# Performance work log

Measured on AMD Instinct MI355X. Metric: run time of the kernel, lower is better.

## Reference

```python
import jax, jax.numpy as jnp
import numpy as np

B = 1024
D = 128  # in_out_dim


def _lin(k, i, o):
    return jax.random.normal(k, (i, o), jnp.float32) / np.sqrt(i)


def setup_inputs() -> dict:
    key = jax.random.key(0)
    ks = jax.random.split(key, 24)
    inp = {
        'pseudo_t': jax.random.uniform(ks[0], (), jnp.float32),
        'x': jax.random.normal(ks[1], (B, D), jnp.float32),
        'g_x': jax.random.normal(ks[2], (B, 1), jnp.float32),
        'p': jax.random.uniform(ks[3], (B, 1), jnp.float32),
        # GRN encoder: 128->1024->960->896 (Tanh), decoder 896->128
        'gw0': _lin(ks[4], 128, 1024), 'gb0': jnp.zeros((1024,), jnp.float32),
        'gw1': _lin(ks[5], 1024, 960), 'gb1': jnp.zeros((960,), jnp.float32),
        'gw2': _lin(ks[6], 960, 896), 'gb2': jnp.zeros((896,), jnp.float32),
        'gdw': _lin(ks[7], 896, 128), 'gdb': jnp.zeros((128,), jnp.float32),
        # BRD encoder: 129->512->448 (Tanh), decoder 448->1
        'bw0': _lin(ks[8], 129, 512), 'bb0': jnp.zeros((512,), jnp.float32),
        'bw1': _lin(ks[9], 512, 448), 'bb1': jnp.zeros((448,), jnp.float32),
        'bdw': _lin(ks[10], 448, 1), 'bdb': jnp.zeros((1,), jnp.float32),
    }
    return inp


def reference(pseudo_t, x, g_x, p, gw0, gb0, gw1, gb1, gw2, gb2, gdw, gdb,
              bw0, bb0, bw1, bb1, bdw, bdb):
    bsz = x.shape[0]
    x_gene = x[:, :-1]                       # [B, D-1]
    s = jnp.full((bsz, 1), pseudo_t, x.dtype)

    def grn(state):                          # [..., D] -> [..., D]
        h = jnp.tanh(state @ gw0 + gb0)
        h = jnp.tanh(h @ gw1 + gb1)
        h = jnp.tanh(h @ gw2 + gb2)
        return h @ gdw + gdb

    dx_dt = grn(jnp.concatenate([s, x_gene], axis=1))   # [B, D]

    # BRD growth function g(x, t)
    st = jnp.concatenate([s, x], axis=1)                # [B, D+1]
    e = jnp.tanh(st @ bw0 + bb0)
    e = jnp.tanh(e @ bw1 + bb1)
    g = e @ bdw + bdb                                   # [B, 1]

    # trace of d(dx_dt[:, :D-1]) / d(x_gene), per sample (CNF divergence)
    s_scalar = jnp.reshape(pseudo_t, (1,)).astype(x.dtype)

    def f_single(xg_i):                                 # [D-1] -> [D]
        return grn(jnp.concatenate([s_scalar, xg_i]))

    jac = jax.vmap(jax.jacfwd(f_single))(x_gene)        # [B, D, D-1]
    tr = jnp.trace(jac[:, :D - 1, :], axis1=1, axis2=2) # [B]

    dp_dt = g - p * tr[:, None]                         # [B, 1]
    return (dx_dt, g, dp_dt)
```

## Files before the change

kernel.cpp:

```cpp
#include <hip/hip_runtime.h>


typedef __bf16 bf16;
typedef __bf16 bf16x8 __attribute__((ext_vector_type(8)));
typedef float floatx4 __attribute__((ext_vector_type(4)));

#if defined(__has_builtin)
#if __has_builtin(__builtin_amdgcn_global_load_lds)
#define HAVE_GLL 1
#endif
#endif

typedef __attribute__((address_space(3))) char lds_char_t;
typedef __attribute__((address_space(1))) const char gbl_char_t;

__device__ inline void async_load16(const void* gp, void* lp) {
#ifdef HAVE_GLL
  __builtin_amdgcn_global_load_lds((gbl_char_t*)gp, (lds_char_t*)lp, 16, 0, 0);
#else
  *(bf16x8*)lp = *(const bf16x8*)gp;
#endif
}

__device__ inline void stage_async(const bf16* src, long row0, int ld, int kc,
                                   bf16* dst, int wid, int sr8, int cph) {
#pragma unroll
  for (int t = 0; t < 4; ++t) {
    const int r = (wid * 4 + t) * 8 + sr8;
    const int csrc = (cph - r) & 7;
    async_load16(src + (row0 + r) * (size_t)ld + kc + csrc * 8,
                 dst + r * 64 + cph * 8);
  }
}

__device__ inline void mfma_block(const bf16* As, const bf16* Bs,
                                  floatx4 (&acc)[4][4], int wm, int wn,
                                  int l16, int quad) {
#pragma unroll
  for (int ks = 0; ks < 2; ++ks) {
    bf16x8 af[4], bfv[4];
#pragma unroll
    for (int mt = 0; mt < 4; ++mt) {
      const int r = wm * 64 + mt * 16 + l16;
      const int c = (ks * 4 + quad + r) & 7;
      af[mt] = *(const bf16x8*)(As + r * 64 + c * 8);
    }
#pragma unroll
    for (int nt = 0; nt < 4; ++nt) {
      const int r = wn * 64 + nt * 16 + l16;
      const int c = (ks * 4 + quad + r) & 7;
      bfv[nt] = *(const bf16x8*)(Bs + r * 64 + c * 8);
    }
#pragma unroll
    for (int mt = 0; mt < 4; ++mt)
#pragma unroll
      for (int nt = 0; nt < 4; ++nt)
        acc[mt][nt] = __builtin_amdgcn_mfma_f32_16x16x32_bf16(af[mt], bfv[nt], acc[mt][nt], 0, 0, 0);
  }
}

__device__ inline void g0_body(bf16* G0, const bf16* gw0b, const bf16* d0b,
                               int i0, int ch, int b, int tid) {
  const int nb = ((b >> 9) << 3) + (b & 7);
  const int inner = (b >> 3) & 63;
  if (nb >= ch) return;
  const int e = inner * 256 + tid;
  const int d = e >> 7;
  const int j = (e & 127) << 3;
  const int ig = i0 + nb;
  const int wsel = (d + 1 < 128) ? d + 1 : 127;
  bf16x8 gv = *(const bf16x8*)(gw0b + wsel * 1024 + j);
  bf16x8 dv = *(const bf16x8*)(d0b + (size_t)ig * 1024 + j);
  bf16x8 v;
#pragma unroll
  for (int k = 0; k < 8; ++k) v[k] = (bf16)((float)gv[k] * (float)dv[k]);
  *(bf16x8*)(G0 + ((size_t)nb * 128 + d) * 1024 + j) = v;
}

struct T8 {
  const bf16* A;
  const bf16* Bm;
  const bf16* sc;
  bf16* Upr;
  const float* gdw;
  float* tr;
  int i0, NT, ch, nTiles;
  int chn, i0n;
  bf16* G0;
  const bf16* gw0b;
  const bf16* d0b;
};

__device__ __forceinline__ void gemm256(const bf16* Aop, const bf16* Bop,
                                        int m0, int n0, int NT, char* lds,
                                        floatx4 (&acc)[8][4]) {
  const int tid = threadIdx.x;
  const int wid = tid >> 6, lane = tid & 63;
  const int wm = wid & 1, wn = wid >> 1;
  const int quad = lane >> 4, l16 = lane & 15;

  const int sr = tid >> 2;
  const int sg = tid & 3;
  const int gs = sg ^ (sr & 3);
  const bf16* aS0 = Aop + (size_t)(m0 + sr) * 1024 + gs * 8;
  const bf16* aS1 = aS0 + (size_t)128 * 1024;
  const bf16* bS0 = Bop + (size_t)(n0 + sr) * 1024 + gs * 8;
  const bf16* bS1 = bS0 + (size_t)128 * 1024;
  const int dO0 = tid * 16, dO1 = 8192 + tid * 16;

  const int fsw = (quad ^ (l16 & 3)) * 8;
  const int fo  = (wm * 128 + l16) * 32 + fsw;
  const int fob = (wn * 64  + l16) * 32 + fsw;

#define STAGE_PAIR(tt, ss)                                                     \
  {                                                                            \
    char* db = lds + (((tt) & 1) * 65536) + ((ss) * 16384);                    \
    const int kc = (tt) * 64 + (ss) * 32;                                      \
    async_load16(aS0 + kc, db + dO0);                                          \
    async_load16(aS1 + kc, db + dO1);                                          \
    async_load16(bS0 + kc, db + 32768 + dO0);                                  \
    async_load16(bS1 + kc, db + 32768 + dO1);                                  \
  }

#define PHASE(T, S, DOSTAGE, ST, SS, VMSEL)                                    \
  {                                                                            \
    const bf16* Af = (const bf16*)(lds + ((T) & 1) * 65536 + (S) * 16384) + fo;\
    const bf16* Bf = (const bf16*)(lds + ((T) & 1) * 65536 + 32768 +           \
                                   (S) * 16384) + fob;                         \
    bf16x8 af[8], bv[4];                                                       \
    _Pragma("unroll")                                                          \
    for (int mf = 0; mf < 8; ++mf) af[mf] = *(const bf16x8*)(Af + mf * 512);   \
    _Pragma("unroll")                                                          \
    for (int nf = 0; nf < 4; ++nf) bv[nf] = *(const bf16x8*)(Bf + nf * 512);   \
    if (DOSTAGE) STAGE_PAIR(ST, SS);                                           \
    __builtin_amdgcn_sched_barrier(0);                                         \
    {                                                                          \
      const int vms = (VMSEL);                                                 \
      if (vms == 8)      asm volatile("s_waitcnt vmcnt(8)");                   \
      else if (vms == 4) asm volatile("s_waitcnt vmcnt(4)");                   \
      else if (vms == 0) asm volatile("s_waitcnt vmcnt(0)");                   \
    }                                                                          \
    __builtin_amdgcn_sched_barrier(0);                                         \
    __builtin_amdgcn_s_setprio(1);                                             \
    _Pragma("unroll")                                                          \
    for (int mf = 0; mf < 8; ++mf)                                             \
      _Pragma("unroll")                                                        \
      for (int nf = 0; nf < 4; ++nf)                                           \
        acc[mf][nf] = __builtin_amdgcn_mfma_f32_16x16x32_bf16(                 \
            af[mf], bv[nf], acc[mf][nf], 0, 0, 0);                             \
    __builtin_amdgcn_s_setprio(0);                                             \
    asm volatile("s_waitcnt lgkmcnt(0)");                                      \
    __builtin_amdgcn_sched_barrier(0);                                         \
    __builtin_amdgcn_s_barrier();                                              \
    __builtin_amdgcn_sched_barrier(0);                                         \
  }

  STAGE_PAIR(0, 0);
  STAGE_PAIR(0, 1);
  STAGE_PAIR(1, 0);
  __builtin_amdgcn_sched_barrier(0);
  asm volatile("s_waitcnt vmcnt(8)");
  __builtin_amdgcn_sched_barrier(0);
  __builtin_amdgcn_s_barrier();
  __builtin_amdgcn_sched_barrier(0);

#pragma unroll 2
  for (int t = 0; t < NT; ++t) {
    PHASE(t, 0, (t + 1 < NT), t + 1, 1, (t + 1 < NT) ? 8 : 0);
    PHASE(t, 1, (t + 2 < NT), t + 2, 0,
          (t + 2 < NT) ? 8 : ((t + 1 < NT) ? 4 : -1));
  }
#undef PHASE
#undef STAGE_PAIR
}

__global__ __launch_bounds__(512, 2) void kt8_b1(T8 p) {
  extern __shared__ __align__(16) char lds[];
  const int mt = (blockIdx.x >> 3) & 3;
  const int nt = ((blockIdx.x >> 5) << 3) | (blockIdx.x & 7);
  if (nt >= p.nTiles) return;

  floatx4 acc[8][4];
#pragma unroll
  for (int a = 0; a < 8; ++a)
#pragma unroll
    for (int b = 0; b < 4; ++b)
#pragma unroll
      for (int r = 0; r < 4; ++r) acc[a][b][r] = 0.0f;

  gemm256(p.A, p.Bm, mt * 256, nt * 256, p.NT, lds, acc);

  const int tid = threadIdx.x;
  const int wid = tid >> 6, lane = tid & 63;
  const int wm = wid & 1, wn = wid >> 1;
  const int quad = lane >> 4, l16 = lane & 15;
  const long nLim = (long)p.ch * 128;
  const int mb = mt * 256 + wm * 128;

#pragma unroll
  for (int nf = 0; nf < 4; ++nf) {
    const long n = (long)nt * 256 + wn * 64 + nf * 16 + l16;
    if (n < nLim) {
      const int ig = p.i0 + (int)(n >> 7);
      const bf16* dp = p.sc + (size_t)ig * 960;
      bf16* urow = p.Upr + (size_t)n * 1024;
#pragma unroll
      for (int mf = 0; mf < 8; ++mf) {
        const int mg = mb + mf * 16 + quad * 4;
        if (mg < 960) {
          union { bf16 h[4]; uint2 u; } o;
#pragma unroll
          for (int r = 0; r < 4; ++r)
            o.h[r] = (bf16)(acc[mf][nf][r] * (float)dp[mg + r]);
          *(uint2*)(urow + mg) = o.u;
        }
      }
    }
  }
}

__global__ __launch_bounds__(512, 2) void kt8_b2(T8 p) {
  extern __shared__ __align__(16) char lds[];
  const int mt = (blockIdx.x >> 3) & 3;
  const int nt = ((blockIdx.x >> 5) << 3) | (blockIdx.x & 7);
  const int tid = threadIdx.x;

  if (nt < p.nTiles) {
    floatx4 acc[8][4];
#pragma unroll
    for (int a = 0; a < 8; ++a)
#pragma unroll
      for (int b = 0; b < 4; ++b)
#pragma unroll
        for (int r = 0; r < 4; ++r) acc[a][b][r] = 0.0f;

    gemm256(p.A, p.Bm, mt * 256, nt * 256, p.NT, lds, acc);

    const int wid = tid >> 6, lane = tid & 63;
    const int wm = wid & 1, wn = wid >> 1;
    const int quad = lane >> 4, l16 = lane & 15;
    const long nLim = (long)p.ch * 128;
    const int mb = mt * 256 + wm * 128;

    float s = 0.0f;
#pragma unroll
    for (int nf = 0; nf < 4; ++nf) {
      const long n = (long)nt * 256 + wn * 64 + nf * 16 + l16;
      const int d = (int)(n & 127);
      if (n < nLim && d < 127) {
        const int ig = p.i0 + (int)(n >> 7);
        const bf16* dp = p.sc + (size_t)ig * 896;
#pragma unroll
        for (int mf = 0; mf < 8; ++mf) {
          const int mg = mb + mf * 16 + quad * 4;
          if (mg < 896) {
#pragma unroll
            for (int r = 0; r < 4; ++r) {
              const float w = (float)dp[mg + r] * p.gdw[(mg + r) * 128 + d];
              s += acc[mf][nf][r] * w;
            }
          }
        }
      }
    }
#pragma unroll
    for (int off = 1; off < 64; off <<= 1) s += __shfl_xor(s, off, 64);
    float* red = (float*)lds;
    if (lane == 0) red[wid] = s;
    __syncthreads();
    const int igA = p.i0 + nt * 2;
    if (tid == 0)
      atomicAdd(p.tr + igA, red[0] + red[1] + red[2] + red[3]);
    if (tid == 256 && nt * 2 + 1 < p.ch)
      atomicAdd(p.tr + igA + 1, red[4] + red[5] + red[6] + red[7]);
  }

  if (p.chn > 0) {
    const size_t V = (size_t)p.chn * 16384;
    for (size_t v = (size_t)blockIdx.x * 512 + tid; v < V;
         v += (size_t)gridDim.x * 512) {
      const int j = ((int)(v & 127)) << 3;
      const size_t rest = v >> 7;
      const int d = (int)(rest & 127);
      const int nb = (int)(rest >> 7);
      const int wsel = (d + 1 < 128) ? d + 1 : 127;
      bf16x8 gv = *(const bf16x8*)(p.gw0b + wsel * 1024 + j);
      bf16x8 dv = *(const bf16x8*)(p.d0b + (size_t)(p.i0n + nb) * 1024 + j);
      bf16x8 o;
#pragma unroll
      for (int k = 0; k < 8; ++k) o[k] = (bf16)((float)gv[k] * (float)dv[k]);
      *(bf16x8*)(p.G0 + ((size_t)nb * 128 + d) * 1024 + j) = o;
    }
  }
}

struct FArgs {
  const bf16* A; int lda;
  const bf16* Bt; int ldb;
  const float* bias;
  bf16* C; int ldc;
  bf16* D; int ldd;
  float* outF; int ldo;
  int K; int realN; int gridX;
};

template <int ACT>
__device__ inline void fwd_body(const FArgs& p, int bx, bf16* As, bf16* Bs) {
  const int tid  = threadIdx.x;
  const int wid  = tid >> 6, lane = tid & 63;
  const int wm   = wid & 1, wn = wid >> 1;
  const int quad = lane >> 4, l16 = lane & 15;
  const int sr8  = lane >> 3, cph = lane & 7;
  const int m0   = (bx % p.gridX) * 128;
  const int bn0  = (bx / p.gridX) * 128;

  floatx4 acc[4][4];
#pragma unroll
  for (int a = 0; a < 4; ++a)
#pragma unroll
    for (int b = 0; b < 4; ++b)
#pragma unroll
      for (int r = 0; r < 4; ++r) acc[a][b][r] = 0.0f;

  for (int kc = 0; kc < p.K; kc += 64) {
    stage_async(p.A, m0, p.lda, kc, As, wid, sr8, cph);
    stage_async(p.Bt, bn0, p.ldb, kc, Bs, wid, sr8, cph);
    __syncthreads();
    mfma_block(As, Bs, acc, wm, wn, l16, quad);
    __syncthreads();
  }

#pragma unroll
  for (int nt = 0; nt < 4; ++nt) {
    const int ng = bn0 + wn * 64 + nt * 16 + l16;
    const float bv = (ng < p.realN) ? p.bias[ng] : 0.0f;
#pragma unroll
    for (int mt = 0; mt < 4; ++mt)
#pragma unroll
      for (int r = 0; r < 4; ++r) {
        const int i = m0 + wm * 64 + mt * 16 + quad * 4 + r;
        const float v = acc[mt][nt][r] + bv;
        if (ACT) {
          const float t = tanhf(v);
          p.C[(size_t)i * p.ldc + ng] = (ng < p.realN) ? (bf16)t : (bf16)0.0f;
          if (p.D && ng < p.realN)
            p.D[(size_t)i * p.ldd + ng] = (bf16)(1.0f - t * t);
        } else if (ng < p.realN) {
          p.outF[(size_t)i * p.ldo + ng] = v;
        }
      }
  }
}

__global__ __launch_bounds__(256) void kt_fwd2(FArgs a, int na, FArgs b) {
  __shared__ __align__(16) bf16 As[8192];
  __shared__ __align__(16) bf16 Bs[8192];
  const int bx = blockIdx.x;
  if (bx < na) fwd_body<1>(a, bx, As, Bs);
  else         fwd_body<1>(b, bx - na, As, Bs);
}

__global__ __launch_bounds__(256) void kt_l2g0(FArgs a, int na, bf16* G0,
                                               const bf16* gw0b, const bf16* d0b,
                                               int i0, int ch) {
  __shared__ __align__(16) bf16 As[8192];
  __shared__ __align__(16) bf16 Bs[8192];
  const int bx = blockIdx.x;
  if (bx < na) fwd_body<1>(a, bx, As, Bs);
  else         g0_body(G0, gw0b, d0b, i0, ch, bx - na, threadIdx.x);
}

__global__ __launch_bounds__(256) void kt_dxgdot(FArgs a, int na,
                                                 const bf16* e1b, const float* bdw,
                                                 const float* bdb, float* gf,
                                                 float* gout) {
  __shared__ __align__(16) bf16 As[8192];
  __shared__ __align__(16) bf16 Bs[8192];
  const int bx = blockIdx.x;
  if (bx < na) { fwd_body<0>(a, bx, As, Bs); return; }
  const int i = (bx - na) * 4 + (threadIdx.x >> 6);
  const int lane = threadIdx.x & 63;
  float s = 0.0f;
  for (int k = lane; k < 448; k += 64) s += (float)e1b[(size_t)i * 512 + k] * bdw[k];
#pragma unroll
  for (int off = 32; off > 0; off >>= 1) s += __shfl_down(s, off, 64);
  if (lane == 0) {
    const float v = s + bdb[0];
    gf[i] = v;
    gout[i] = v;
  }
}

struct PArgs {
  const float *gw0, *gw1, *gw2, *gdw, *bw0, *bw1, *pt, *x;
  bf16 *gw0b, *gw0t, *gw1t, *gw2t, *gdwt, *bw0t, *bw1t, *Xg, *Xb;
};

__device__ inline void tpose_tile(bf16* dst, const float* src, int R, int C,
                                  int ldd, int tile, int tilesX, float* tl,
                                  int tid) {
  const int r0 = (tile % tilesX) * 64;
  const int c0 = (tile / tilesX) * 64;
  const int tx = tid & 63, ty0 = tid >> 6;
#pragma unroll
  for (int i = 0; i < 16; ++i) {
    const int ty = ty0 + i * 4;
    const int r = r0 + ty, c = c0 + tx;
    tl[ty * 65 + tx] = (r < R && c < C) ? src[(size_t)r * C + c] : 0.0f;
  }
  __syncthreads();
#pragma unroll
  for (int i = 0; i < 16; ++i) {
    const int ty = ty0 + i * 4;
    dst[(size_t)(c0 + ty) * ldd + r0 + tx] = (bf16)tl[tx * 65 + ty];
  }
}

__global__ __launch_bounds__(256) void kt_prep(PArgs p) {
  __shared__ float tl[64 * 65];
  int b = blockIdx.x;
  const int t = threadIdx.x;
  if (b < 512) { p.gw0b[b * 256 + t] = (bf16)p.gw0[b * 256 + t]; return; }
  b -= 512;
  if (b < 768) {
    const int idx = b * 256 + t;
    const int i = idx / 192, c = idx % 192;
    const float s = p.pt[0];
    float vb;
    if (c == 0) vb = s;
    else if (c <= 128) vb = p.x[i * 128 + c - 1];
    else vb = 0.0f;
    p.Xb[i * 192 + c] = (bf16)vb;
    if (c < 128) p.Xg[i * 128 + c] = (bf16)((c == 0) ? s : p.x[i * 128 + c - 1]);
    return;
  }
  b -= 768;
  if (b < 32)  { tpose_tile(p.gw0t, p.gw0, 128, 1024, 128, b, 2, tl, t);  return; }
  b -= 32;
  if (b < 256) { tpose_tile(p.gw1t, p.gw1, 1024, 960, 1024, b, 16, tl, t); return; }
  b -= 256;
  if (b < 256) { tpose_tile(p.gw2t, p.gw2, 960, 896, 1024, b, 16, tl, t); return; }
  b -= 256;
  if (b < 32)  { tpose_tile(p.gdwt, p.gdw, 896, 128, 1024, b, 16, tl, t); return; }
  b -= 32;
  if (b < 24)  { tpose_tile(p.bw0t, p.bw0, 129, 512, 192, b, 3, tl, t);  return; }
  b -= 24;
  if (b < 64)  { tpose_tile(p.bw1t, p.bw1, 512, 448, 512, b, 8, tl, t);  return; }
}

__global__ __launch_bounds__(256) void kt_fin(const float* gf, const float* tr,
                                              const float* pp, float* dp) {
  const int i = blockIdx.x * 256 + threadIdx.x;
  if (i < 1024) dp[i] = gf[i] - pp[i] * tr[i];
}

extern "C" void kernel_launch(void* const* d_in, const int* in_sizes, int n_in,
                              void* d_out, int out_size, void* d_ws, size_t ws_size,
                              hipStream_t stream) {
  const float* pt  = (const float*)d_in[0];
  const float* x   = (const float*)d_in[1];
  const float* pp  = (const float*)d_in[3];
  const float* gw0 = (const float*)d_in[4];
  const float* gb0 = (const float*)d_in[5];
  const float* gw1 = (const float*)d_in[6];
  const float* gb1 = (const float*)d_in[7];
  const float* gw2 = (const float*)d_in[8];
  const float* gb2 = (const float*)d_in[9];
  const float* gdw = (const float*)d_in[10];
  const float* gdb = (const float*)d_in[11];
  const float* bw0 = (const float*)d_in[12];
  const float* bb0 = (const float*)d_in[13];
  const float* bw1 = (const float*)d_in[14];
  const float* bb1 = (const float*)d_in[15];
  const float* bdw = (const float*)d_in[16];
  const float* bdb = (const float*)d_in[17];
  float* out = (float*)d_out;

  static bool s_attr = false;
  if (!s_attr) {
    hipFuncSetAttribute((const void*)kt8_b1,
                        hipFuncAttributeMaxDynamicSharedMemorySize, 131072);
    hipFuncSetAttribute((const void*)kt8_b2,
                        hipFuncAttributeMaxDynamicSharedMemorySize, 131072);
    s_attr = true;
  }

  char* w = (char*)d_ws;
  size_t used = 0;
  auto alloc = [&](size_t nbytes) -> void* {
    void* r = w + used;
    used += (nbytes + 255) & ~(size_t)255;
    return r;
  };
  bf16* gw0b = (bf16*)alloc((size_t)128 * 1024 * 2);
  bf16* gw0t = (bf16*)alloc((size_t)1024 * 128 * 2);
  bf16* gw1t = (bf16*)alloc((size_t)1024 * 1024 * 2);
  bf16* gw2t = (bf16*)alloc((size_t)1024 * 1024 * 2);
  bf16* gdwt = (bf16*)alloc((size_t)128 * 1024 * 2);
  bf16* bw0t = (bf16*)alloc((size_t)512 * 192 * 2);
  bf16* bw1t = (bf16*)alloc((size_t)512 * 512 * 2);
  bf16* Xg   = (bf16*)alloc((size_t)1024 * 128 * 2);
  bf16* Xb   = (bf16*)alloc((size_t)1024 * 192 * 2);
  bf16* h0b  = (bf16*)alloc((size_t)1024 * 1024 * 2);
  bf16* h1b  = (bf16*)alloc((size_t)1024 * 1024 * 2);
  bf16* h2b  = (bf16*)alloc((size_t)1024 * 1024 * 2);
  bf16* e0b  = (bf16*)alloc((size_t)1024 * 512 * 2);
  bf16* e1b  = (bf16*)alloc((size_t)1024 * 512 * 2);
  bf16* d0b  = (bf16*)alloc((size_t)1024 * 1024 * 2);
  bf16* d1b  = (bf16*)alloc((size_t)1024 * 960 * 2);
  bf16* d2b  = (bf16*)alloc((size_t)1024 * 896 * 2);
  float* gf  = (float*)alloc(1024 * 4);
  float* tr  = (float*)alloc(1024 * 4);

  const size_t perSample = (size_t)128 * 1024 * 2;
  size_t avail = (ws_size > used) ? ws_size - used : 0;
  int CH = (int)(avail / (2 * perSample));
  if (CH > 256) CH = 256;
  if (CH >= 2) CH &= ~1;
  if (CH < 1) CH = 1;
  bf16* G0  = (bf16*)alloc((size_t)CH * perSample);
  bf16* Upr = (bf16*)(w + used);

  hipMemsetAsync(tr, 0, 1024 * 4, stream);

  {
    PArgs a{gw0, gw1, gw2, gdw, bw0, bw1, pt, x,
            gw0b, gw0t, gw1t, gw2t, gdwt, bw0t, bw1t, Xg, Xb};
    kt_prep<<<dim3(1944), 256, 0, stream>>>(a);
  }

  {
    FArgs a{}; a.A = Xg; a.lda = 128; a.Bt = gw0t; a.ldb = 128; a.bias = gb0;
    a.C = h0b; a.ldc = 1024; a.D = d0b; a.ldd = 1024; a.K = 128; a.realN = 1024;
    a.gridX = 8;
    FArgs b{}; b.A = Xb; b.lda = 192; b.Bt = bw0t; b.ldb = 192; b.bias = bb0;
    b.C = e0b; b.ldc = 512; b.K = 192; b.realN = 512; b.gridX = 8;
    kt_fwd2<<<dim3(96), 256, 0, stream>>>(a, 64, b);
  }
  {
    FArgs a{}; a.A = h0b; a.lda = 1024; a.Bt = gw1t; a.ldb = 1024; a.bias = gb1;
    a.C = h1b; a.ldc = 1024; a.D = d1b; a.ldd = 960; a.K = 1024; a.realN = 960;
    a.gridX = 8;
    FArgs b{}; b.A = e0b; b.lda = 512; b.Bt = bw1t; b.ldb = 512; b.bias = bb1;
    b.C = e1b; b.ldc = 512; b.K = 512; b.realN = 448; b.gridX = 8;
    kt_fwd2<<<dim3(96), 256, 0, stream>>>(a, 64, b);
  }
  const int ch0  = (1024 < CH) ? 1024 : CH;
  const int ch08 = (ch0 + 7) & ~7;
  {
    FArgs a{}; a.A = h1b; a.lda = 1024; a.Bt = gw2t; a.ldb = 1024; a.bias = gb2;
    a.C = h2b; a.ldc = 1024; a.D = d2b; a.ldd = 896; a.K = 1024; a.realN = 896;
    a.gridX = 8;
    kt_l2g0<<<dim3(56 + ch08 * 64), 256, 0, stream>>>(a, 56, G0, gw0b, d0b, 0, ch0);
  }
  {
    FArgs a{}; a.A = h2b; a.lda = 1024; a.Bt = gdwt; a.ldb = 1024; a.bias = gdb;
    a.outF = out; a.ldo = 128; a.K = 896; a.realN = 128; a.gridX = 8;
    kt_dxgdot<<<dim3(8 + 256), 256, 0, stream>>>(a, 8, e1b, bdw, bdb, gf, out + 131072);
  }

  for (int i0 = 0; i0 < 1024; i0 += CH) {
    const int ch  = (1024 - i0 < CH) ? (1024 - i0) : CH;
    const int nTiles = (ch * 128 + 255) >> 8;
    const int nT8 = (nTiles + 7) & ~7;
    {
      T8 a{}; a.A = gw1t; a.Bm = G0; a.sc = d1b; a.Upr = Upr; a.i0 = i0;
      a.NT = 16; a.ch = ch; a.nTiles = nTiles;
      kt8_b1<<<dim3(nT8 * 4), 512, 131072, stream>>>(a);
    }
    {
      const int i0n = i0 + CH;
      const int chn = (i0n < 1024) ? ((1024 - i0n < CH) ? (1024 - i0n) : CH) : 0;
      T8 a{}; a.A = gw2t; a.Bm = Upr; a.sc = d2b; a.gdw = gdw; a.tr = tr;
      a.i0 = i0; a.NT = 15; a.ch = ch; a.nTiles = nTiles;
      a.chn = chn; a.i0n = i0n; a.G0 = G0; a.gw0b = gw0b; a.d0b = d0b;
      kt8_b2<<<dim3(nT8 * 4), 512, 131072, stream>>>(a);
    }
  }

  kt_fin<<<dim3(4), 256, 0, stream>>>(gf, tr, pp, out + 132096);
}
```

Measured before the change: 805.0 us.

## Restructure 256x256 GEMM mainloop into quadrant-interleaved LDS reads and MFMA phases

Replaces the two-half-K-step staging, which used 32-wide K slices with an XOR swizzle, with one 64-wide K tile per stage. The new LDS layout uses a rotation swizzle, and each iteration is split into four quadrant phases (A-half x B-half) so that LDS fragment reads for the next quadrant overlap the barriers and MFMAs of the current one. The aim is to cut register pressure and LDS read stalls while keeping a double-buffered global-to-LDS prefetch. In exchange it adds more barriers per iteration and a full vmcnt(0) wait at the end of each tile, which reduces the prefetch lookahead.

```diff
diff --git a/kernel.cpp b/kernel.cpp
--- a/kernel.cpp
+++ b/kernel.cpp
@@ -99,79 +99,114 @@
   const int wm = wid & 1, wn = wid >> 1;
   const int quad = lane >> 4, l16 = lane & 15;
 
-  const int sr = tid >> 2;
-  const int sg = tid & 3;
-  const int gs = sg ^ (sr & 3);
-  const bf16* aS0 = Aop + (size_t)(m0 + sr) * 1024 + gs * 8;
-  const bf16* aS1 = aS0 + (size_t)128 * 1024;
-  const bf16* bS0 = Bop + (size_t)(n0 + sr) * 1024 + gs * 8;
-  const bf16* bS1 = bS0 + (size_t)128 * 1024;
-  const int dO0 = tid * 16, dO1 = 8192 + tid * 16;
-
-  const int fsw = (quad ^ (l16 & 3)) * 8;
-  const int fo  = (wm * 128 + l16) * 32 + fsw;
-  const int fob = (wn * 64  + l16) * 32 + fsw;
-
-#define STAGE_PAIR(tt, ss)                                                     \
+  const int sr = tid >> 3;
+  const int sg = tid & 7;
+  const int csrc = (sg - sr) & 7;
+  const bf16* aSrc = Aop + (size_t)(m0 + sr) * 1024 + csrc * 8;
+  const bf16* bSrc = Bop + (size_t)(n0 + sr) * 1024 + csrc * 8;
+
+  const int rA = wm * 128 + l16;
+  const int rB = wn * 64 + l16;
+  const int aO0 = rA * 64 + ((quad + rA) & 7) * 8;
+  const int aO1 = rA * 64 + ((4 + quad + rA) & 7) * 8;
+  const int bO0 = rB * 64 + ((quad + rB) & 7) * 8;
+  const int bO1 = rB * 64 + ((4 + quad + rB) & 7) * 8;
+
+#define STAGE8(tt)                                                             \
   {                                                                            \
-    char* db = lds + (((tt) & 1) * 65536) + ((ss) * 16384);                    \
-    const int kc = (tt) * 64 + (ss) * 32;                                      \
-    async_load16(aS0 + kc, db + dO0);                                          \
-    async_load16(aS1 + kc, db + dO1);                                          \
-    async_load16(bS0 + kc, db + 32768 + dO0);                                  \
-    async_load16(bS1 + kc, db + 32768 + dO1);                                  \
-  }
-
-#define PHASE(T, S, DOSTAGE, ST, SS, VMSEL)                                    \
-  {                                                                            \
-    const bf16* Af = (const bf16*)(lds + ((T) & 1) * 65536 + (S) * 16384) + fo;\
-    const bf16* Bf = (const bf16*)(lds + ((T) & 1) * 65536 + 32768 +           \
-                                   (S) * 16384) + fob;                         \
-    bf16x8 af[8], bv[4];                                                       \
+    char* db = lds + (((tt) & 1) * 65536);                                     \
+    const int kc2 = (tt) * 64;                                                 \
     _Pragma("unroll")                                                          \
-    for (int mf = 0; mf < 8; ++mf) af[mf] = *(const bf16x8*)(Af + mf * 512);   \
+    for (int q = 0; q < 4; ++q)                                                \
+      async_load16(aSrc + (size_t)q * 65536 + kc2, db + q * 8192 + tid * 16);  \
     _Pragma("unroll")                                                          \
-    for (int nf = 0; nf < 4; ++nf) bv[nf] = *(const bf16x8*)(Bf + nf * 512);   \
-    if (DOSTAGE) STAGE_PAIR(ST, SS);                                           \
-    __builtin_amdgcn_sched_barrier(0);                                         \
-    {                                                                          \
-      const int vms = (VMSEL);                                                 \
-      if (vms == 8)      asm volatile("s_waitcnt vmcnt(8)");                   \
-      else if (vms == 4) asm volatile("s_waitcnt vmcnt(4)");                   \
-      else if (vms == 0) asm volatile("s_waitcnt vmcnt(0)");                   \
+    for (int q = 0; q < 4; ++q)                                                \
+      async_load16(bSrc + (size_t)q * 65536 + kc2,                             \
+                   db + 32768 + q * 8192 + tid * 16);                          \
+  }
+
+#define READ_A(MH)                                                             \
+  _Pragma("unroll")                                                            \
+  for (int mf = 0; mf < 4; ++mf) {                                             \
+    aA[mf] = *(const bf16x8*)(BA + aO0 + ((MH) * 4 + mf) * 1024);              \
+    aB[mf] = *(const bf16x8*)(BA + aO1 + ((MH) * 4 + mf) * 1024);              \
+  }
+
+#define READ_B(NH)                                                             \
+  _Pragma("unroll")                                                            \
+  for (int nf = 0; nf < 2; ++nf) {                                             \
+    bA[nf] = *(const bf16x8*)(BB + bO0 + ((NH) * 2 + nf) * 1024);              \
+    bB[nf] = *(const bf16x8*)(BB + bO1 + ((NH) * 2 + nf) * 1024);              \
+  }
+
+#define MFMA16(MH, NH)                                                         \
+  __builtin_amdgcn_s_setprio(1);                                               \
+  _Pragma("unroll")                                                            \
+  for (int mf = 0; mf < 4; ++mf)                                               \
+    _Pragma("unroll")                                                          \
+    for (int nf = 0; nf < 2; ++nf) {                                           \
+      acc[(MH) * 4 + mf][(NH) * 2 + nf] =                                      \
+          __builtin_amdgcn_mfma_f32_16x16x32_bf16(                             \
+              aA[mf], bA[nf], acc[(MH) * 4 + mf][(NH) * 2 + nf], 0, 0, 0);     \
+      acc[(MH) * 4 + mf][(NH) * 2 + nf] =                                      \
+          __builtin_amdgcn_mfma_f32_16x16x32_bf16(                             \
+              aB[mf], bB[nf], acc[(MH) * 4 + mf][(NH) * 2 + nf], 0, 0, 0);     \
     }                                                                          \
-    __builtin_amdgcn_sched_barrier(0);                                         \
-    __builtin_amdgcn_s_setprio(1);                                             \
-    _Pragma("unroll")                                                          \
-    for (int mf = 0; mf < 8; ++mf)                                             \
-      _Pragma("unroll")                                                        \
-      for (int nf = 0; nf < 4; ++nf)                                           \
-        acc[mf][nf] = __builtin_amdgcn_mfma_f32_16x16x32_bf16(                 \
-            af[mf], bv[nf], acc[mf][nf], 0, 0, 0);                             \
-    __builtin_amdgcn_s_setprio(0);                                             \
-    asm volatile("s_waitcnt lgkmcnt(0)");                                      \
-    __builtin_amdgcn_sched_barrier(0);                                         \
-    __builtin_amdgcn_s_barrier();                                              \
-    __builtin_amdgcn_sched_barrier(0);                                         \
-  }
-
-  STAGE_PAIR(0, 0);
-  STAGE_PAIR(0, 1);
-  STAGE_PAIR(1, 0);
+  __builtin_amdgcn_s_setprio(0);
+
+#define BAR_A                                                                  \
+  __builtin_amdgcn_sched_barrier(0);                                           \
+  __builtin_amdgcn_s_barrier();                                                \
+  asm volatile("s_waitcnt lgkmcnt(0)");                                        \
   __builtin_amdgcn_sched_barrier(0);
-  asm volatile("s_waitcnt vmcnt(8)");
+
+#define BAR_B                                                                  \
+  __builtin_amdgcn_sched_barrier(0);                                           \
+  __builtin_amdgcn_s_barrier();                                                \
+  __builtin_amdgcn_sched_barrier(0);
+
+  STAGE8(0);
+  __builtin_amdgcn_sched_barrier(0);
+  asm volatile("s_waitcnt vmcnt(0)");
   __builtin_amdgcn_sched_barrier(0);
   __builtin_amdgcn_s_barrier();
   __builtin_amdgcn_sched_barrier(0);
 
-#pragma unroll 2
   for (int t = 0; t < NT; ++t) {
-    PHASE(t, 0, (t + 1 < NT), t + 1, 1, (t + 1 < NT) ? 8 : 0);
-    PHASE(t, 1, (t + 2 < NT), t + 2, 0,
-          (t + 2 < NT) ? 8 : ((t + 1 < NT) ? 4 : -1));
-  }
-#undef PHASE
-#undef STAGE_PAIR
+    const bf16* BA = (const bf16*)(lds + (t & 1) * 65536);
+    const bf16* BB = BA + 16384;
+    bf16x8 aA[4], aB[4], bA[2], bB[2];
+
+    READ_A(0);
+    READ_B(0);
+    if (t + 1 < NT) STAGE8(t + 1);
+    BAR_A;
+    MFMA16(0, 0);
+    BAR_B;
+
+    READ_B(1);
+    BAR_A;
+    MFMA16(0, 1);
+    BAR_B;
+
+    READ_A(1);
+    BAR_A;
+    MFMA16(1, 1);
+    BAR_B;
+
+    READ_B(0);
+    BAR_A;
+    MFMA16(1, 0);
+    __builtin_amdgcn_sched_barrier(0);
+    asm volatile("s_waitcnt vmcnt(0)");
+    BAR_B;
+  }
+#undef STAGE8
+#undef READ_A
+#undef READ_B
+#undef MFMA16
+#undef BAR_A
+#undef BAR_B
 }
 
 __global__ __launch_bounds__(512, 2) void kt8_b1(T8 p) {
```

After: 832.5 us. +3.4%, slower.

## Restructure gemm256 into a four-slot LDS ring with a rotated swizzle

Applied to the files above, without the earlier changes.

Replaces the double-buffered two-phase pipeline with a four-slot ring of half-K LDS buffers. Each half-step issues the async global-to-LDS loads two slots ahead and then computes, with one vmcnt wait and a barrier per half-step. It also drops the per-phase setprio, lgkmcnt wait and sched_barriers. The XOR swizzle becomes a rotation-based one (quad + row>>1) to avoid LDS bank conflicts under the new 64-byte row layout. The deeper prefetch is meant to hide global latency better, at the risk of ordering hazards now that the explicit lgkmcnt wait is gone.

```diff
diff --git a/kernel.cpp b/kernel.cpp
--- a/kernel.cpp
+++ b/kernel.cpp
@@ -101,77 +101,74 @@
 
   const int sr = tid >> 2;
   const int sg = tid & 3;
-  const int gs = sg ^ (sr & 3);
-  const bf16* aS0 = Aop + (size_t)(m0 + sr) * 1024 + gs * 8;
-  const bf16* aS1 = aS0 + (size_t)128 * 1024;
-  const bf16* bS0 = Bop + (size_t)(n0 + sr) * 1024 + gs * 8;
-  const bf16* bS1 = bS0 + (size_t)128 * 1024;
-  const int dO0 = tid * 16, dO1 = 8192 + tid * 16;
-
-  const int fsw = (quad ^ (l16 & 3)) * 8;
-  const int fo  = (wm * 128 + l16) * 32 + fsw;
-  const int fob = (wn * 64  + l16) * 32 + fsw;
-
-#define STAGE_PAIR(tt, ss)                                                     \
+  const int csrc = (sg - (sr >> 1)) & 3;
+  const bf16* aSrc = Aop + (size_t)(m0 + sr) * 1024 + csrc * 8;
+  const bf16* bSrc = Bop + (size_t)(n0 + sr) * 1024 + csrc * 8;
+
+  const int rA = wm * 128 + l16;
+  const int rB = wn * 64 + l16;
+  const int aOff = rA * 64 + ((quad + (rA >> 1)) & 3) * 16;
+  const int bOff = rB * 64 + ((quad + (rB >> 1)) & 3) * 16;
+
+#define STAGE4(hh)                                                             \
   {                                                                            \
-    char* db = lds + (((tt) & 1) * 65536) + ((ss) * 16384);                    \
-    const int kc = (tt) * 64 + (ss) * 32;                                      \
-    async_load16(aS0 + kc, db + dO0);                                          \
-    async_load16(aS1 + kc, db + dO1);                                          \
-    async_load16(bS0 + kc, db + 32768 + dO0);                                  \
-    async_load16(bS1 + kc, db + 32768 + dO1);                                  \
-  }
-
-#define PHASE(T, S, DOSTAGE, ST, SS, VMSEL)                                    \
+    char* db = lds + ((hh) & 3) * 32768;                                       \
+    const int kce = (hh) * 32;                                                 \
+    async_load16(aSrc + kce, db + tid * 16);                                   \
+    async_load16(aSrc + 131072 + kce, db + 8192 + tid * 16);                   \
+    async_load16(bSrc + kce, db + 16384 + tid * 16);                           \
+    async_load16(bSrc + 131072 + kce, db + 24576 + tid * 16);                  \
+  }
+
+#define HALF_COMPUTE(HB)                                                       \
   {                                                                            \
-    const bf16* Af = (const bf16*)(lds + ((T) & 1) * 65536 + (S) * 16384) + fo;\
-    const bf16* Bf = (const bf16*)(lds + ((T) & 1) * 65536 + 32768 +           \
-                                   (S) * 16384) + fob;                         \
+    const char* hb_ = (const char*)(HB);                                       \
     bf16x8 af[8], bv[4];                                                       \
     _Pragma("unroll")                                                          \
-    for (int mf = 0; mf < 8; ++mf) af[mf] = *(const bf16x8*)(Af + mf * 512);   \
+    for (int nf = 0; nf < 4; ++nf)                                             \
+      bv[nf] = *(const bf16x8*)(hb_ + 16384 + bOff + nf * 1024);               \
     _Pragma("unroll")                                                          \
-    for (int nf = 0; nf < 4; ++nf) bv[nf] = *(const bf16x8*)(Bf + nf * 512);   \
-    if (DOSTAGE) STAGE_PAIR(ST, SS);                                           \
-    __builtin_amdgcn_sched_barrier(0);                                         \
-    {                                                                          \
-      const int vms = (VMSEL);                                                 \
-      if (vms == 8)      asm volatile("s_waitcnt vmcnt(8)");                   \
-      else if (vms == 4) asm volatile("s_waitcnt vmcnt(4)");                   \
-      else if (vms == 0) asm volatile("s_waitcnt vmcnt(0)");                   \
-    }                                                                          \
-    __builtin_amdgcn_sched_barrier(0);                                         \
-    __builtin_amdgcn_s_setprio(1);                                             \
+    for (int mf = 0; mf < 8; ++mf)                                             \
+      af[mf] = *(const bf16x8*)(hb_ + aOff + mf * 1024);                       \
     _Pragma("unroll")                                                          \
     for (int mf = 0; mf < 8; ++mf)                                             \
       _Pragma("unroll")                                                        \
       for (int nf = 0; nf < 4; ++nf)                                           \
         acc[mf][nf] = __builtin_amdgcn_mfma_f32_16x16x32_bf16(                 \
             af[mf], bv[nf], acc[mf][nf], 0, 0, 0);                             \
-    __builtin_amdgcn_s_setprio(0);                                             \
-    asm volatile("s_waitcnt lgkmcnt(0)");                                      \
-    __builtin_amdgcn_sched_barrier(0);                                         \
-    __builtin_amdgcn_s_barrier();                                              \
-    __builtin_amdgcn_sched_barrier(0);                                         \
-  }
-
-  STAGE_PAIR(0, 0);
-  STAGE_PAIR(0, 1);
-  STAGE_PAIR(1, 0);
-  __builtin_amdgcn_sched_barrier(0);
-  asm volatile("s_waitcnt vmcnt(8)");
-  __builtin_amdgcn_sched_barrier(0);
-  __builtin_amdgcn_s_barrier();
-  __builtin_amdgcn_sched_barrier(0);
+  }
+
+#define VMW(N) asm volatile("s_waitcnt vmcnt(" #N ")" ::: "memory")
+#define BARRIER()                                                              \
+  asm volatile("s_barrier" ::: "memory");                                      \
+  __builtin_amdgcn_sched_barrier(0)
+
+  STAGE4(0);
+  STAGE4(1);
+  VMW(4);
+  BARRIER();
 
 #pragma unroll 2
   for (int t = 0; t < NT; ++t) {
-    PHASE(t, 0, (t + 1 < NT), t + 1, 1, (t + 1 < NT) ? 8 : 0);
-    PHASE(t, 1, (t + 2 < NT), t + 2, 0,
-          (t + 2 < NT) ? 8 : ((t + 1 < NT) ? 4 : -1));
-  }
-#undef PHASE
-#undef STAGE_PAIR
+    const int h0 = 2 * t;
+    const bool more = (t + 1 < NT);
+
+    if (more) STAGE4(h0 + 2);
+    HALF_COMPUTE(lds + (h0 & 3) * 32768);
+    if (more) VMW(4); else VMW(0);
+    BARRIER();
+
+    if (more) STAGE4(h0 + 3);
+    HALF_COMPUTE(lds + ((h0 + 1) & 3) * 32768);
+    if (more) {
+      VMW(4);
+      BARRIER();
+    }
+  }
+#undef STAGE4
+#undef HALF_COMPUTE
+#undef VMW
+#undef BARRIER
 }
 
 __global__ __launch_bounds__(512, 2) void kt8_b1(T8 p) {
```

Result: slower. 881.4 us (+9.5%).
